# Performance work log

Measured on AMD Instinct MI355X. Metric: run time of the kernel, lower is better.

The kernel has to match this reference:

```python
import jax, jax.numpy as jnp
import numpy as np

NUM_EXPERTS = 64
NUM_SELECTED = 2
HASH_BITS = 32


def setup_inputs() -> dict:
    key = jax.random.key(0)
    k1, k2 = jax.random.split(key)
    hidden_states = jax.random.normal(k1, (4, 4096, 2048), dtype=jnp.float32)
    # torch Linear weight [out_features, in_features], init normal(std=0.01), bias zeros
    hash_w = jax.random.normal(k2, (NUM_SELECTED * HASH_BITS, 2048), dtype=jnp.float32) * 0.01
    hash_b = jnp.zeros((NUM_SELECTED * HASH_BITS,), dtype=jnp.float32)
    return {"hidden_states": hidden_states, "hash_w": hash_w, "hash_b": hash_b}


def reference(hidden_states, hash_w, hash_b):
    B, S, H = hidden_states.shape
    T = B * S
    x = hidden_states.reshape(T, H)
    # hash projection: [T, k*32]
    h = x @ hash_w.T + hash_b
    bits = (h > 0).astype(jnp.int32).reshape(T, NUM_SELECTED, HASH_BITS)
    cand = bits.sum(axis=-1) % NUM_EXPERTS  # [T, k] candidate expert per slot

    # Sequential dedup (vectorized over tokens): for each slot i in order, if the
    # candidate collides with an already-chosen expert for that token, advance
    # (e+1) % E until a free expert is found (always exists since k <= E).
    used = jnp.zeros((T, NUM_EXPERTS), dtype=bool)
    offs = jnp.arange(NUM_EXPERTS)
    chosen = []
    for i in range(NUM_SELECTED):
        e = cand[:, i]  # [T]
        pos = (e[:, None] + offs[None, :]) % NUM_EXPERTS  # [T, E] probe sequence
        probed = jnp.take_along_axis(used, pos, axis=1)  # [T, E] used flags along probe
        off = jnp.argmax(~probed, axis=1)  # first free offset (0 if candidate free)
        ne = (e + off) % NUM_EXPERTS
        used = used | jax.nn.one_hot(ne, NUM_EXPERTS, dtype=bool)
        chosen.append(ne)
    expert_indices = jnp.stack(chosen, axis=1).astype(jnp.int32)  # [T, k]
    expert_weights = jnp.full((T, NUM_SELECTED), 1.0 / NUM_SELECTED, dtype=jnp.float32)
    router_logits = jnp.zeros((T, NUM_EXPERTS), dtype=jnp.float32)
    return expert_weights, expert_indices, router_logits
```

## Files before the change

kernel.cpp:

```cpp
#include <hip/hip_runtime.h>


typedef __attribute__((ext_vector_type(8))) short short8;
typedef __attribute__((ext_vector_type(4))) float f32x4;

constexpr int H    = 2048;
constexpr int NJ   = 64;
constexpr int TOKB = 64;
constexpr int KC   = 128;
constexpr int NCH  = H / KC;
constexpr int RS   = 136;
constexpr int PL   = TOKB * RS;

__device__ __forceinline__ unsigned short bf16_rne(float f) {
    unsigned u = __float_as_uint(f);
    u += 0x7fffu + ((u >> 16) & 1u);
    return (unsigned short)(u >> 16);
}
__device__ __forceinline__ void split1(float f, unsigned short& h, unsigned short& l) {
    h = bf16_rne(f);
    const float hf = __uint_as_float((unsigned)h << 16);
    l = bf16_rne(f - hf);
}

__global__ __launch_bounds__(256) void wcvt_kernel(
    const float* __restrict__ w, unsigned short* __restrict__ wh,
    unsigned short* __restrict__ wl) {
    const int i = (blockIdx.x * 256 + threadIdx.x) * 4;
    const float4 v = *(const float4*)(w + i);
    ushort4 h, l;
    split1(v.x, h.x, l.x); split1(v.y, h.y, l.y);
    split1(v.z, h.z, l.z); split1(v.w, h.w, l.w);
    *(ushort4*)(wh + i) = h;
    *(ushort4*)(wl + i) = l;
}

__global__ __launch_bounds__(512, 2) void hash_router_kernel(
    const float* __restrict__ x,
    const float* __restrict__ w,
    const float* __restrict__ b,
    const unsigned short* __restrict__ wh,
    const unsigned short* __restrict__ wl,
    float* __restrict__ out,
    int T)
{
    __shared__ unsigned short smem[2 * 2 * PL];
    __shared__ int cnt[TOKB][2];

    const int tid  = threadIdx.x;
    const int lane = tid & 63;
    const int wv   = tid >> 6;
    const int tg   = wv & 3;
    const int nh   = wv >> 1 & 2 ? 0 : 0;
    (void)nh;
    const int nhalf = wv >> 2;
    const int tok0 = blockIdx.x * TOKB;
    const int l15  = lane & 15;
    const int quad = lane >> 4;

    f32x4 acc[2] = {{0.f, 0.f, 0.f, 0.f}, {0.f, 0.f, 0.f, 0.f}};

    float4 stg[4];
#pragma unroll
    for (int it = 0; it < 4; ++it) {
        const int s = it * 512 + tid;
        const int row = s >> 5, c4 = s & 31;
        stg[it] = *(const float4*)(x + (size_t)(tok0 + row) * H + c4 * 4);
    }

    for (int ch = 0; ch < NCH; ++ch) {
        const int bb = (ch & 1) * 2 * PL;
#pragma unroll
        for (int it = 0; it < 4; ++it) {
            const int s = it * 512 + tid;
            const int row = s >> 5, c4 = s & 31;
            const float4 v = stg[it];
            ushort4 h, l;
            split1(v.x, h.x, l.x); split1(v.y, h.y, l.y);
            split1(v.z, h.z, l.z); split1(v.w, h.w, l.w);
            *(ushort4*)(smem + bb + row * RS + c4 * 4)      = h;
            *(ushort4*)(smem + bb + PL + row * RS + c4 * 4) = l;
        }
        if (ch + 1 < NCH) {
#pragma unroll
            for (int it = 0; it < 4; ++it) {
                const int s = it * 512 + tid;
                const int row = s >> 5, c4 = s & 31;
                stg[it] = *(const float4*)(x + (size_t)(tok0 + row) * H + (ch + 1) * KC + c4 * 4);
            }
        }
        __syncthreads();

        const unsigned short* ab = smem + bb + (tg * 16 + l15) * RS + quad * 8;
#pragma unroll
        for (int ks = 0; ks < 4; ++ks) {
            const short8 ah = *(const short8*)(ab + ks * 32);
            const short8 al = *(const short8*)(ab + PL + ks * 32);
#pragma unroll
            for (int nt = 0; nt < 2; ++nt) {
                const size_t wo = (size_t)(nhalf * 32 + nt * 16 + l15) * H + ch * KC + ks * 32 + quad * 8;
                const short8 bh = *(const short8*)(wh + wo);
                const short8 bl = *(const short8*)(wl + wo);
                acc[nt] = __builtin_amdgcn_mfma_f32_16x16x32_bf16(ah, bh, acc[nt], 0, 0, 0);
                acc[nt] = __builtin_amdgcn_mfma_f32_16x16x32_bf16(al, bh, acc[nt], 0, 0, 0);
                acc[nt] = __builtin_amdgcn_mfma_f32_16x16x32_bf16(ah, bl, acc[nt], 0, 0, 0);
            }
        }
    }

    float bias[2];
#pragma unroll
    for (int nt = 0; nt < 2; ++nt) bias[nt] = b[nhalf * 32 + nt * 16 + l15];

    bool pos[2][4];
#pragma unroll
    for (int nt = 0; nt < 2; ++nt)
#pragma unroll
        for (int r = 0; r < 4; ++r) {
            const float v = acc[nt][r] + bias[nt];
            bool p;
            if (__builtin_expect(fabsf(v) < 5e-5f, 0)) {
                const int t = tok0 + tg * 16 + quad * 4 + r;
                const int j = nhalf * 32 + nt * 16 + l15;
                const float* xr = x + (size_t)t * H;
                const float* wr = w + (size_t)j * H;
                double sd = (double)bias[nt];
                for (int k = 0; k < H; ++k)
                    sd += (double)xr[k] * (double)wr[k];
                p = (sd > 0.0);
            } else {
                p = (v > 0.0f);
            }
            pos[nt][r] = p;
        }

    unsigned long long m0[4], m1[4];
#pragma unroll
    for (int r = 0; r < 4; ++r) m0[r] = __ballot(pos[0][r]);
#pragma unroll
    for (int r = 0; r < 4; ++r) m1[r] = __ballot(pos[1][r]);

    if (lane < 16) {
        const int q = lane >> 2, rr = lane & 3;
        const int c = __popcll((m0[rr] >> (q * 16)) & 0xffffull)
                    + __popcll((m1[rr] >> (q * 16)) & 0xffffull);
        cnt[tg * 16 + lane][nhalf] = c;
    }
    __syncthreads();

    if (tid < TOKB) {
        const int t  = tok0 + tid;
        const int c0 = cnt[tid][0];
        const int c1 = cnt[tid][1];
        const int i1 = c1 + ((c1 == c0) ? 1 : 0);
        float2 wq; wq.x = 0.5f; wq.y = 0.5f;
        *(float2*)(out + 2 * (size_t)t) = wq;
        float2 iq; iq.x = (float)c0; iq.y = (float)i1;
        *(float2*)(out + 2 * (size_t)T + 2 * (size_t)t) = iq;
    }

    float4 z; z.x = 0.f; z.y = 0.f; z.z = 0.f; z.w = 0.f;
    float* lbase = out + 4 * (size_t)T + (size_t)tok0 * NJ;
    *(float4*)(lbase + tid * 4) = z;
    *(float4*)(lbase + (tid + 512) * 4) = z;
}

extern "C" void kernel_launch(void* const* d_in, const int* in_sizes, int n_in,
                              void* d_out, int out_size, void* d_ws, size_t ws_size,
                              hipStream_t stream) {
    const float* x = (const float*)d_in[0];
    const float* w = (const float*)d_in[1];
    const float* b = (const float*)d_in[2];
    float* out = (float*)d_out;
    const int T = in_sizes[0] / H;
    unsigned short* wh = (unsigned short*)d_ws;
    unsigned short* wl = wh + NJ * H;

    wcvt_kernel<<<dim3(NJ * H / 1024), dim3(256), 0, stream>>>(w, wh, wl);
    hash_router_kernel<<<dim3(T / TOKB), dim3(512), 0, stream>>>(
        x, w, b, wh, wl, out, T);
}
```

Baseline: 329.4 us.

## Split K across waves with direct global A loads and LDS reduction

Rewrites the router GEMM so each 256-thread block handles 16 tokens. Each of its four waves covers a quarter of the hidden dimension across all 64 outputs. Activations are loaded straight from global memory into registers and split into bf16 hi/lo there, which removes the shared-memory staging and the per-chunk barriers. Partial sums are combined through LDS by wave 0, which then does the sign/popcount epilogue. This yields four times more blocks for better occupancy and latency hiding, at the cost of uncoalesced-ish per-lane x loads and more weight re-reads from L2 per token.

```diff
diff --git a/kernel.cpp b/kernel.cpp
--- a/kernel.cpp
+++ b/kernel.cpp
@@ -6,11 +6,7 @@
 
 constexpr int H    = 2048;
 constexpr int NJ   = 64;
-constexpr int TOKB = 64;
-constexpr int KC   = 128;
-constexpr int NCH  = H / KC;
-constexpr int RS   = 136;
-constexpr int PL   = TOKB * RS;
+constexpr int TOKB = 16;
 
 __device__ __forceinline__ unsigned short bf16_rne(float f) {
     unsigned u = __float_as_uint(f);
@@ -35,7 +31,7 @@
     *(ushort4*)(wl + i) = l;
 }
 
-__global__ __launch_bounds__(512, 2) void hash_router_kernel(
+__global__ __launch_bounds__(256, 4) void hash_router_kernel(
     const float* __restrict__ x,
     const float* __restrict__ w,
     const float* __restrict__ b,
@@ -44,125 +40,114 @@
     float* __restrict__ out,
     int T)
 {
-    __shared__ unsigned short smem[2 * 2 * PL];
-    __shared__ int cnt[TOKB][2];
+    __shared__ float red[3][64][17];
 
     const int tid  = threadIdx.x;
     const int lane = tid & 63;
-    const int wv   = tid >> 6;
-    const int tg   = wv & 3;
-    const int nh   = wv >> 1 & 2 ? 0 : 0;
-    (void)nh;
-    const int nhalf = wv >> 2;
-    const int tok0 = blockIdx.x * TOKB;
+    const int q    = __builtin_amdgcn_readfirstlane(tid >> 6);
     const int l15  = lane & 15;
     const int quad = lane >> 4;
+    const int tok0 = blockIdx.x * TOKB;
 
-    f32x4 acc[2] = {{0.f, 0.f, 0.f, 0.f}, {0.f, 0.f, 0.f, 0.f}};
+    f32x4 acc[4] = {{0.f,0.f,0.f,0.f},{0.f,0.f,0.f,0.f},
+                    {0.f,0.f,0.f,0.f},{0.f,0.f,0.f,0.f}};
 
-    float4 stg[4];
+    const float* xbase = x + (size_t)(tok0 + l15) * H + q * 512 + quad * 8;
+
+#pragma unroll 4
+    for (int ks = 0; ks < 16; ++ks) {
+        const int kb = ks * 32;
+        const float4 a0 = *(const float4*)(xbase + kb);
+        const float4 a1 = *(const float4*)(xbase + kb + 4);
+
+        short8 ah, al;
+        {
+            unsigned short h0,l0,h1,l1,h2,l2,h3,l3;
+            split1(a0.x,h0,l0); split1(a0.y,h1,l1); split1(a0.z,h2,l2); split1(a0.w,h3,l3);
+            ah[0]=(short)h0; ah[1]=(short)h1; ah[2]=(short)h2; ah[3]=(short)h3;
+            al[0]=(short)l0; al[1]=(short)l1; al[2]=(short)l2; al[3]=(short)l3;
+            split1(a1.x,h0,l0); split1(a1.y,h1,l1); split1(a1.z,h2,l2); split1(a1.w,h3,l3);
+            ah[4]=(short)h0; ah[5]=(short)h1; ah[6]=(short)h2; ah[7]=(short)h3;
+            al[4]=(short)l0; al[5]=(short)l1; al[6]=(short)l2; al[7]=(short)l3;
+        }
+
 #pragma unroll
-    for (int it = 0; it < 4; ++it) {
-        const int s = it * 512 + tid;
-        const int row = s >> 5, c4 = s & 31;
-        stg[it] = *(const float4*)(x + (size_t)(tok0 + row) * H + c4 * 4);
-    }
-
-    for (int ch = 0; ch < NCH; ++ch) {
-        const int bb = (ch & 1) * 2 * PL;
-#pragma unroll
-        for (int it = 0; it < 4; ++it) {
-            const int s = it * 512 + tid;
-            const int row = s >> 5, c4 = s & 31;
-            const float4 v = stg[it];
-            ushort4 h, l;
-            split1(v.x, h.x, l.x); split1(v.y, h.y, l.y);
-            split1(v.z, h.z, l.z); split1(v.w, h.w, l.w);
-            *(ushort4*)(smem + bb + row * RS + c4 * 4)      = h;
-            *(ushort4*)(smem + bb + PL + row * RS + c4 * 4) = l;
-        }
-        if (ch + 1 < NCH) {
-#pragma unroll
-            for (int it = 0; it < 4; ++it) {
-                const int s = it * 512 + tid;
-                const int row = s >> 5, c4 = s & 31;
-                stg[it] = *(const float4*)(x + (size_t)(tok0 + row) * H + (ch + 1) * KC + c4 * 4);
-            }
-        }
-        __syncthreads();
-
-        const unsigned short* ab = smem + bb + (tg * 16 + l15) * RS + quad * 8;
-#pragma unroll
-        for (int ks = 0; ks < 4; ++ks) {
-            const short8 ah = *(const short8*)(ab + ks * 32);
-            const short8 al = *(const short8*)(ab + PL + ks * 32);
-#pragma unroll
-            for (int nt = 0; nt < 2; ++nt) {
-                const size_t wo = (size_t)(nhalf * 32 + nt * 16 + l15) * H + ch * KC + ks * 32 + quad * 8;
-                const short8 bh = *(const short8*)(wh + wo);
-                const short8 bl = *(const short8*)(wl + wo);
-                acc[nt] = __builtin_amdgcn_mfma_f32_16x16x32_bf16(ah, bh, acc[nt], 0, 0, 0);
-                acc[nt] = __builtin_amdgcn_mfma_f32_16x16x32_bf16(al, bh, acc[nt], 0, 0, 0);
-                acc[nt] = __builtin_amdgcn_mfma_f32_16x16x32_bf16(ah, bl, acc[nt], 0, 0, 0);
-            }
+        for (int nt = 0; nt < 4; ++nt) {
+            const size_t wo = (size_t)(nt * 16 + l15) * H + q * 512 + kb + quad * 8;
+            const short8 bh = *(const short8*)(wh + wo);
+            const short8 bl = *(const short8*)(wl + wo);
+            acc[nt] = __builtin_amdgcn_mfma_f32_16x16x32_bf16(ah, bh, acc[nt], 0, 0, 0);
+            acc[nt] = __builtin_amdgcn_mfma_f32_16x16x32_bf16(al, bh, acc[nt], 0, 0, 0);
+            acc[nt] = __builtin_amdgcn_mfma_f32_16x16x32_bf16(ah, bl, acc[nt], 0, 0, 0);
         }
     }
 
-    float bias[2];
+    if (q) {
 #pragma unroll
-    for (int nt = 0; nt < 2; ++nt) bias[nt] = b[nhalf * 32 + nt * 16 + l15];
-
-    bool pos[2][4];
+        for (int nt = 0; nt < 4; ++nt)
 #pragma unroll
-    for (int nt = 0; nt < 2; ++nt)
-#pragma unroll
-        for (int r = 0; r < 4; ++r) {
-            const float v = acc[nt][r] + bias[nt];
-            bool p;
-            if (__builtin_expect(fabsf(v) < 5e-5f, 0)) {
-                const int t = tok0 + tg * 16 + quad * 4 + r;
-                const int j = nhalf * 32 + nt * 16 + l15;
-                const float* xr = x + (size_t)t * H;
-                const float* wr = w + (size_t)j * H;
-                double sd = (double)bias[nt];
-                for (int k = 0; k < H; ++k)
-                    sd += (double)xr[k] * (double)wr[k];
-                p = (sd > 0.0);
-            } else {
-                p = (v > 0.0f);
-            }
-            pos[nt][r] = p;
-        }
-
-    unsigned long long m0[4], m1[4];
-#pragma unroll
-    for (int r = 0; r < 4; ++r) m0[r] = __ballot(pos[0][r]);
-#pragma unroll
-    for (int r = 0; r < 4; ++r) m1[r] = __ballot(pos[1][r]);
-
-    if (lane < 16) {
-        const int q = lane >> 2, rr = lane & 3;
-        const int c = __popcll((m0[rr] >> (q * 16)) & 0xffffull)
-                    + __popcll((m1[rr] >> (q * 16)) & 0xffffull);
-        cnt[tg * 16 + lane][nhalf] = c;
+            for (int r = 0; r < 4; ++r)
+                red[q - 1][lane][nt * 4 + r] = acc[nt][r];
     }
     __syncthreads();
 
-    if (tid < TOKB) {
-        const int t  = tok0 + tid;
-        const int c0 = cnt[tid][0];
-        const int c1 = cnt[tid][1];
-        const int i1 = c1 + ((c1 == c0) ? 1 : 0);
-        float2 wq; wq.x = 0.5f; wq.y = 0.5f;
-        *(float2*)(out + 2 * (size_t)t) = wq;
-        float2 iq; iq.x = (float)c0; iq.y = (float)i1;
-        *(float2*)(out + 2 * (size_t)T + 2 * (size_t)t) = iq;
+    if (q == 0) {
+#pragma unroll
+        for (int i = 0; i < 3; ++i)
+#pragma unroll
+            for (int nt = 0; nt < 4; ++nt)
+#pragma unroll
+                for (int r = 0; r < 4; ++r)
+                    acc[nt][r] += red[i][lane][nt * 4 + r];
+
+        bool pos[4][4];
+#pragma unroll
+        for (int nt = 0; nt < 4; ++nt) {
+            const float bias = b[nt * 16 + l15];
+#pragma unroll
+            for (int r = 0; r < 4; ++r) {
+                const float v = acc[nt][r] + bias;
+                bool p;
+                if (__builtin_expect(fabsf(v) < 5e-5f, 0)) {
+                    const int t = tok0 + quad * 4 + r;
+                    const int j = nt * 16 + l15;
+                    const float* xr = x + (size_t)t * H;
+                    const float* wr = w + (size_t)j * H;
+                    double sd = (double)bias;
+                    for (int k = 0; k < H; ++k)
+                        sd += (double)xr[k] * (double)wr[k];
+                    p = (sd > 0.0);
+                } else {
+                    p = (v > 0.0f);
+                }
+                pos[nt][r] = p;
+            }
+        }
+
+        unsigned long long m[4][4];
+#pragma unroll
+        for (int nt = 0; nt < 4; ++nt)
+#pragma unroll
+            for (int r = 0; r < 4; ++r)
+                m[nt][r] = __ballot(pos[nt][r]);
+
+        if (lane < 16) {
+            const int qq = lane >> 2, rr = lane & 3;
+            const int c0 = __popcll((m[0][rr] >> (qq * 16)) & 0xffffull)
+                         + __popcll((m[1][rr] >> (qq * 16)) & 0xffffull);
+            const int c1 = __popcll((m[2][rr] >> (qq * 16)) & 0xffffull)
+                         + __popcll((m[3][rr] >> (qq * 16)) & 0xffffull);
+            const int t  = tok0 + lane;
+            const int i1 = c1 + ((c1 == c0) ? 1 : 0);
+            float2 wq; wq.x = 0.5f; wq.y = 0.5f;
+            *(float2*)(out + 2 * (size_t)t) = wq;
+            float2 iq; iq.x = (float)c0; iq.y = (float)i1;
+            *(float2*)(out + 2 * (size_t)T + 2 * (size_t)t) = iq;
+        }
     }
 
     float4 z; z.x = 0.f; z.y = 0.f; z.z = 0.f; z.w = 0.f;
-    float* lbase = out + 4 * (size_t)T + (size_t)tok0 * NJ;
-    *(float4*)(lbase + tid * 4) = z;
-    *(float4*)(lbase + (tid + 512) * 4) = z;
+    *(float4*)(out + 4 * (size_t)T + (size_t)tok0 * NJ + tid * 4) = z;
 }
 
 extern "C" void kernel_launch(void* const* d_in, const int* in_sizes, int n_in,
@@ -177,6 +162,6 @@
     unsigned short* wl = wh + NJ * H;
 
     wcvt_kernel<<<dim3(NJ * H / 1024), dim3(256), 0, stream>>>(w, wh, wl);
-    hash_router_kernel<<<dim3(T / TOKB), dim3(512), 0, stream>>>(
+    hash_router_kernel<<<dim3(T / TOKB), dim3(256), 0, stream>>>(
         x, w, b, wh, wl, out, T);
 }
```

Result: faster. 308.3 us (-6.4%).
